# Performance work log

Hardware: AMD Instinct MI355X
Metric: run time of the kernel (lower is better)

The kernel has to match this reference:

```python
import jax, jax.numpy as jnp
import numpy as np

AXIS = 0
INPUT_SHAPE = (50000, 1024)
N_IDX = 131072

def setup_inputs() -> dict:
    key = jax.random.key(0)
    k1, k2 = jax.random.split(key)
    grad_last = jax.random.normal(k1, (N_IDX, INPUT_SHAPE[1]), dtype=jnp.float32)
    indices = jax.random.randint(k2, (N_IDX,), 0, INPUT_SHAPE[0], dtype=jnp.int64)
    return {"grad_last": grad_last, "indices": indices}

def reference(grad_last, indices):
    # Gather backward: scatter-add grad_last slices along AXIS into zeros(INPUT_SHAPE).
    # Equivalent to the torch module's per-index loop, done in one fused scatter-add.
    g = jnp.moveaxis(grad_last, AXIS, 0)  # [n_idx, ...rest]
    out_shape = (INPUT_SHAPE[AXIS],) + g.shape[1:]
    out = jnp.zeros(out_shape, dtype=grad_last.dtype).at[indices].add(g)
    return jnp.moveaxis(out, 0, AXIS)
```

## Files before the change

### kernel.cpp

```cpp
#include <hip/hip_runtime.h>
#include <hip/hip_bf16.h>


#define NCOLS 1024
#define C4 (NCOLS / 4)
#define CAP 32

__global__ void fill_kernel(const int* __restrict__ idx, int* __restrict__ cnt,
                            int* __restrict__ bucket, int* __restrict__ ovf_list,
                            int* __restrict__ ovf_cnt, int n) {
    int i = blockIdx.x * blockDim.x + threadIdx.x;
    if (i >= n) return;
    int row = idx[i];
    int local = atomicAdd(&cnt[row], 1);
    if (local < CAP) {
        bucket[(size_t)row * CAP + local] = i;
    } else {
        int s = atomicAdd(ovf_cnt, 1);
        ovf_list[s] = i;
    }
}

__global__ __launch_bounds__(256) void gather_kernel(
    const float4* __restrict__ grad, const int* __restrict__ cnt,
    const int* __restrict__ bucket, float4* __restrict__ out, int nrows) {
    int row = blockIdx.x;
    if (row >= nrows) return;
    int tid = threadIdx.x;
    int n = cnt[row];
    if (n > CAP) n = CAP;
    const int* b = bucket + (size_t)row * CAP;
    float4 acc = {0.f, 0.f, 0.f, 0.f};
    for (int k = 0; k < n; ++k) {
        int g = b[k];
        float4 v = grad[(size_t)g * C4 + tid];
        acc.x += v.x; acc.y += v.y; acc.z += v.z; acc.w += v.w;
    }
    out[(size_t)row * C4 + tid] = acc;
}

__global__ __launch_bounds__(256) void overflow_kernel(
    const float4* __restrict__ grad, const int* __restrict__ idx,
    const int* __restrict__ ovf_list, const int* __restrict__ ovf_cnt,
    float* __restrict__ out) {
    int n = *ovf_cnt;
    for (int e = blockIdx.x; e < n; e += gridDim.x) {
        int i = ovf_list[e];
        int row = idx[i];
        float4 v = grad[(size_t)i * C4 + threadIdx.x];
        float* o = out + (size_t)row * NCOLS + (size_t)threadIdx.x * 4;
        atomicAdd(o + 0, v.x);
        atomicAdd(o + 1, v.y);
        atomicAdd(o + 2, v.z);
        atomicAdd(o + 3, v.w);
    }
}

__global__ __launch_bounds__(256) void scatter_atomic_kernel(
    const float4* __restrict__ grad, const int* __restrict__ idx,
    float* __restrict__ out, int n_idx) {
    int row = blockIdx.x;
    if (row >= n_idx) return;
    int c4 = threadIdx.x;
    int target = idx[row];
    float4 v = grad[(size_t)row * C4 + c4];
    float* o = out + (size_t)target * NCOLS + (size_t)c4 * 4;
    atomicAdd(o + 0, v.x);
    atomicAdd(o + 1, v.y);
    atomicAdd(o + 2, v.z);
    atomicAdd(o + 3, v.w);
}

extern "C" void kernel_launch(void* const* d_in, const int* in_sizes, int n_in,
                              void* d_out, int out_size, void* d_ws, size_t ws_size,
                              hipStream_t stream) {
    const float4* grad = (const float4*)d_in[0];
    const int* idx = (const int*)d_in[1];

    int n_idx = in_sizes[1];
    int nrows = out_size / NCOLS;

    size_t need = ((size_t)nrows * (CAP + 1) + 1 + n_idx) * sizeof(int);
    if (ws_size < need) {
        hipMemsetAsync(d_out, 0, (size_t)out_size * sizeof(float), stream);
        scatter_atomic_kernel<<<n_idx, 256, 0, stream>>>(grad, idx, (float*)d_out, n_idx);
        return;
    }

    int* cnt      = (int*)d_ws;
    int* ovf_cnt  = cnt + nrows;
    int* bucket   = ovf_cnt + 1;
    int* ovf_list = bucket + (size_t)nrows * CAP;

    hipMemsetAsync(cnt, 0, ((size_t)nrows + 1) * sizeof(int), stream);

    int blk = 256;
    fill_kernel<<<(n_idx + blk - 1) / blk, blk, 0, stream>>>(
        idx, cnt, bucket, ovf_list, ovf_cnt, n_idx);
    gather_kernel<<<nrows, 256, 0, stream>>>(grad, cnt, bucket,
                                             (float4*)d_out, nrows);
    overflow_kernel<<<128, 256, 0, stream>>>(grad, idx, ovf_list, ovf_cnt,
                                             (float*)d_out);
}
```

Measured before the change: 172.2 us.

## Pack row count and bucket into 64-byte record and batch gather loads

Merges the per-row counter and bucket of source indices into one 16-int record per output row, so the gather kernel reads all metadata with four int4 loads instead of a dependent count read followed by per-iteration bucket reads. The gather loop is fully unrolled over a cap of 15 and issues all row loads before accumulating, which raises memory-level parallelism. The cap drops from 32 to 15, so rows with more than 15 contributions go to the atomic overflow path, and the memset now clears the whole metadata array instead of only the counters. Register use grows with 15 float4 values held per thread.

```diff
diff --git a/kernel.cpp b/kernel.cpp
--- a/kernel.cpp
+++ b/kernel.cpp
@@ -4,17 +4,17 @@
 
 #define NCOLS 1024
 #define C4 (NCOLS / 4)
-#define CAP 32
+#define CAP 15
 
-__global__ void fill_kernel(const int* __restrict__ idx, int* __restrict__ cnt,
-                            int* __restrict__ bucket, int* __restrict__ ovf_list,
-                            int* __restrict__ ovf_cnt, int n) {
+__global__ void fill_kernel(const int* __restrict__ idx, int* __restrict__ meta,
+                            int* __restrict__ ovf_list, int* __restrict__ ovf_cnt,
+                            int n) {
     int i = blockIdx.x * blockDim.x + threadIdx.x;
     if (i >= n) return;
     int row = idx[i];
-    int local = atomicAdd(&cnt[row], 1);
+    int local = atomicAdd(&meta[(size_t)row * 16], 1);
     if (local < CAP) {
-        bucket[(size_t)row * CAP + local] = i;
+        meta[(size_t)row * 16 + 1 + local] = i;
     } else {
         int s = atomicAdd(ovf_cnt, 1);
         ovf_list[s] = i;
@@ -22,20 +22,36 @@
 }
 
 __global__ __launch_bounds__(256) void gather_kernel(
-    const float4* __restrict__ grad, const int* __restrict__ cnt,
-    const int* __restrict__ bucket, float4* __restrict__ out, int nrows) {
+    const float4* __restrict__ grad, const int4* __restrict__ meta4,
+    float4* __restrict__ out, int nrows) {
     int row = blockIdx.x;
     if (row >= nrows) return;
     int tid = threadIdx.x;
-    int n = cnt[row];
+
+    int4 m0 = meta4[(size_t)row * 4 + 0];
+    int4 m1 = meta4[(size_t)row * 4 + 1];
+    int4 m2 = meta4[(size_t)row * 4 + 2];
+    int4 m3 = meta4[(size_t)row * 4 + 3];
+    int n = m0.x;
     if (n > CAP) n = CAP;
-    const int* b = bucket + (size_t)row * CAP;
+    int g[CAP] = {m0.y, m0.z, m0.w,
+                  m1.x, m1.y, m1.z, m1.w,
+                  m2.x, m2.y, m2.z, m2.w,
+                  m3.x, m3.y, m3.z, m3.w};
+
+    float4 v[CAP];
+    #pragma unroll
+    for (int k = 0; k < CAP; ++k)
+        if (k < n) v[k] = grad[(size_t)g[k] * C4 + tid];
+
     float4 acc = {0.f, 0.f, 0.f, 0.f};
-    for (int k = 0; k < n; ++k) {
-        int g = b[k];
-        float4 v = grad[(size_t)g * C4 + tid];
-        acc.x += v.x; acc.y += v.y; acc.z += v.z; acc.w += v.w;
-    }
+    #pragma unroll
+    for (int k = 0; k < CAP; ++k)
+        if (k < n) {
+            acc.x += v[k].x; acc.y += v[k].y;
+            acc.z += v[k].z; acc.w += v[k].w;
+        }
+
     out[(size_t)row * C4 + tid] = acc;
 }
 
@@ -80,24 +96,23 @@
     int n_idx = in_sizes[1];
     int nrows = out_size / NCOLS;
 
-    size_t need = ((size_t)nrows * (CAP + 1) + 1 + n_idx) * sizeof(int);
+    size_t need = ((size_t)nrows * 16 + 1 + n_idx) * sizeof(int);
     if (ws_size < need) {
         hipMemsetAsync(d_out, 0, (size_t)out_size * sizeof(float), stream);
         scatter_atomic_kernel<<<n_idx, 256, 0, stream>>>(grad, idx, (float*)d_out, n_idx);
         return;
     }
 
-    int* cnt      = (int*)d_ws;
-    int* ovf_cnt  = cnt + nrows;
-    int* bucket   = ovf_cnt + 1;
-    int* ovf_list = bucket + (size_t)nrows * CAP;
+    int* meta     = (int*)d_ws;
+    int* ovf_cnt  = meta + (size_t)nrows * 16;
+    int* ovf_list = ovf_cnt + 1;
 
-    hipMemsetAsync(cnt, 0, ((size_t)nrows + 1) * sizeof(int), stream);
+    hipMemsetAsync(meta, 0, ((size_t)nrows * 16 + 1) * sizeof(int), stream);
 
     int blk = 256;
     fill_kernel<<<(n_idx + blk - 1) / blk, blk, 0, stream>>>(
-        idx, cnt, bucket, ovf_list, ovf_cnt, n_idx);
-    gather_kernel<<<nrows, 256, 0, stream>>>(grad, cnt, bucket,
+        idx, meta, ovf_list, ovf_cnt, n_idx);
+    gather_kernel<<<nrows, 256, 0, stream>>>(grad, (const int4*)meta,
                                              (float4*)d_out, nrows);
     overflow_kernel<<<128, 256, 0, stream>>>(grad, idx, ovf_list, ovf_cnt,
                                              (float*)d_out);
```

After: 166.2 us. 1.04x faster.
